# Kernel tuning notes

Measured on AMD Instinct MI355X. Metric: run time of the kernel, lower is better.

The kernel has to match this reference:

```python
import jax, jax.numpy as jnp
import numpy as np

N_NODES = 100000
N_EDGES = 1600000
DIM = 3
HID = 128
BN_EPS = 1e-5


def _bn(x, g, b):
    # BatchNorm1d, training-mode batch statistics (biased variance, like torch)
    m = jnp.mean(x, axis=0)
    v = jnp.var(x, axis=0)
    return (x - m) * jax.lax.rsqrt(v + BN_EPS) * g + b


def _gin_mlp(h, w1, b1, g1, be1, w2, b2, g2, be2, w3, b3):
    # Linear -> BN -> ReLU -> (Dropout: identity in eval) -> Linear -> BN -> ReLU -> Linear
    h = jax.nn.relu(_bn(h @ w1 + b1, g1, be1))
    h = jax.nn.relu(_bn(h @ w2 + b2, g2, be2))
    return h @ w3 + b3


def _gin_conv(x, src, dst, eps, mlp_params):
    # GINConv: mlp((1+eps)*x_i + sum_{j->i} x_j); scatter-add over edge targets
    agg = jax.ops.segment_sum(x[src], dst, num_segments=N_NODES)
    return _gin_mlp((1.0 + eps) * x + agg, *mlp_params)


def setup_inputs() -> dict:
    key = jax.random.key(0)
    ks = jax.random.split(key, 32)

    def w(k, shape, scale=0.05):
        return jax.random.normal(k, shape, dtype=jnp.float32) * scale

    inp = {}
    inp["coords"] = jax.random.normal(ks[0], (N_NODES, DIM), dtype=jnp.float32)
    inp["edge_index"] = jax.random.randint(ks[1], (2, N_EDGES), 0, N_NODES, dtype=jnp.int32)

    # GIN layer 0 MLP (dim -> hid -> hid -> hid)
    inp["g0_w1"] = w(ks[2], (DIM, HID)); inp["g0_b1"] = jnp.zeros((HID,), jnp.float32)
    inp["g0_g1"] = jnp.ones((HID,), jnp.float32); inp["g0_be1"] = jnp.zeros((HID,), jnp.float32)
    inp["g0_w2"] = w(ks[3], (HID, HID)); inp["g0_b2"] = jnp.zeros((HID,), jnp.float32)
    inp["g0_g2"] = jnp.ones((HID,), jnp.float32); inp["g0_be2"] = jnp.zeros((HID,), jnp.float32)
    inp["g0_w3"] = w(ks[4], (HID, HID)); inp["g0_b3"] = jnp.zeros((HID,), jnp.float32)
    inp["eps0"] = jnp.zeros((), jnp.float32)
    inp["bn0_g"] = jnp.ones((HID,), jnp.float32); inp["bn0_b"] = jnp.zeros((HID,), jnp.float32)

    # GIN layer 1 MLP (hid -> hid -> hid -> hid)
    inp["g1_w1"] = w(ks[5], (HID, HID)); inp["g1_b1"] = jnp.zeros((HID,), jnp.float32)
    inp["g1_g1"] = jnp.ones((HID,), jnp.float32); inp["g1_be1"] = jnp.zeros((HID,), jnp.float32)
    inp["g1_w2"] = w(ks[6], (HID, HID)); inp["g1_b2"] = jnp.zeros((HID,), jnp.float32)
    inp["g1_g2"] = jnp.ones((HID,), jnp.float32); inp["g1_be2"] = jnp.zeros((HID,), jnp.float32)
    inp["g1_w3"] = w(ks[7], (HID, HID)); inp["g1_b3"] = jnp.zeros((HID,), jnp.float32)
    inp["eps1"] = jnp.zeros((), jnp.float32)
    inp["bn1_g"] = jnp.ones((HID,), jnp.float32); inp["bn1_b"] = jnp.zeros((HID,), jnp.float32)

    # decoder MLP: (2*hid+1) -> hid -> hid//2 -> 1, sigmoid
    inp["d_w1"] = w(ks[8], (2 * HID + 1, HID)); inp["d_b1"] = jnp.zeros((HID,), jnp.float32)
    inp["d_g"] = jnp.ones((HID,), jnp.float32); inp["d_be"] = jnp.zeros((HID,), jnp.float32)
    inp["d_w2"] = w(ks[9], (HID, HID // 2)); inp["d_b2"] = jnp.zeros((HID // 2,), jnp.float32)
    inp["d_w3"] = w(ks[10], (HID // 2, 1)); inp["d_b3"] = jnp.zeros((1,), jnp.float32)
    return inp


def reference(coords, edge_index,
              g0_w1, g0_b1, g0_g1, g0_be1, g0_w2, g0_b2, g0_g2, g0_be2, g0_w3, g0_b3, eps0, bn0_g, bn0_b,
              g1_w1, g1_b1, g1_g1, g1_be1, g1_w2, g1_b2, g1_g2, g1_be2, g1_w3, g1_b3, eps1, bn1_g, bn1_b,
              d_w1, d_b1, d_g, d_be, d_w2, d_b2, d_w3, d_b3):
    node_0 = edge_index[0]
    node_1 = edge_index[1]

    mlp0 = (g0_w1, g0_b1, g0_g1, g0_be1, g0_w2, g0_b2, g0_g2, g0_be2, g0_w3, g0_b3)
    mlp1 = (g1_w1, g1_b1, g1_g1, g1_be1, g1_w2, g1_b2, g1_g2, g1_be2, g1_w3, g1_b3)

    x = _gin_conv(coords, node_0, node_1, eps0, mlp0)
    x = jax.nn.relu(_bn(x, bn0_g, bn0_b))
    x = _gin_conv(x, node_0, node_1, eps1, mlp1)
    x = jax.nn.relu(_bn(x, bn1_g, bn1_b))

    # edge_l_cntr branch: per-edge contour-length feature + endpoint concat
    l = jnp.linalg.norm(coords[node_1] - coords[node_0], axis=1, keepdims=True)  # [E,1]
    h = jnp.concatenate([x[node_0], x[node_1], l], axis=-1)  # [E, 2*hid+1]

    h = jax.nn.relu(_bn(h @ d_w1 + d_b1, d_g, d_be))
    h = jax.nn.relu(h @ d_w2 + d_b2)
    out = jax.nn.sigmoid((h @ d_w3 + d_b3).squeeze(-1))  # [E]
    return out
```

## Files before the change

### kernel.cpp

```cpp
#include <hip/hip_runtime.h>
#include <hip/hip_bf16.h>
#include <math.h>


typedef __attribute__((ext_vector_type(8))) __bf16 bf16x8;
typedef __attribute__((ext_vector_type(4))) float f32x4;

__device__ __forceinline__ unsigned int pack_bf16(float a, float b) {
    unsigned short ua = __builtin_bit_cast(unsigned short, __float2bfloat16(a));
    unsigned short ub = __builtin_bit_cast(unsigned short, __float2bfloat16(b));
    return (unsigned int)ua | ((unsigned int)ub << 16);
}
__device__ __forceinline__ float bflo(unsigned int u) {
    return __builtin_bit_cast(float, u << 16);
}
__device__ __forceinline__ float bfhi(unsigned int u) {
    return __builtin_bit_cast(float, u & 0xffff0000u);
}
__device__ __forceinline__ unsigned short bf16r(float a) {
    return __builtin_bit_cast(unsigned short, __float2bfloat16(a));
}


__global__ void hist_dst(const int* __restrict__ edst, int* __restrict__ cursor, int E) {
    int e = blockIdx.x * 256 + threadIdx.x;
    if (e < E) atomicAdd(&cursor[edst[e]], 1);
}

__global__ __launch_bounds__(1024) void scan_deg(const int* deg, int* rowoff, int* cursor, int N) {
    __shared__ int sums[1024];
    const int t = threadIdx.x;
    const int chunk = (N + 1023) >> 10;
    int lo = t * chunk, hi = lo + chunk;
    if (lo > N) lo = N;
    if (hi > N) hi = N;
    int s = 0;
    for (int i = lo; i < hi; ++i) s += deg[i];
    sums[t] = s;
    __syncthreads();
    for (int off = 1; off < 1024; off <<= 1) {
        int add = (t >= off) ? sums[t - off] : 0;
        __syncthreads();
        sums[t] += add;
        __syncthreads();
    }
    int run = sums[t] - s;
    for (int i = lo; i < hi; ++i) {
        int d = deg[i];
        rowoff[i] = run;
        cursor[i] = run;
        run += d;
    }
    if (t == 1023) rowoff[N] = sums[1023];
}

__global__ void fill_csr(const int* __restrict__ esrc, const int* __restrict__ edst,
                         const float* __restrict__ coords,
                         int* cursor, int* __restrict__ perm, int* __restrict__ dperm,
                         int* __restrict__ eperm, float* __restrict__ lperm, int E) {
    int e = blockIdx.x * 256 + threadIdx.x;
    if (e >= E) return;
    int s0 = esrc[e], d0 = edst[e];
    int pos = atomicAdd(&cursor[d0], 1);
    perm[pos] = s0;
    dperm[pos] = d0;
    eperm[pos] = e;
    float dx = coords[d0*3+0] - coords[s0*3+0];
    float dy = coords[d0*3+1] - coords[s0*3+1];
    float dz = coords[d0*3+2] - coords[s0*3+2];
    lperm[pos] = sqrtf(dx*dx + dy*dy + dz*dz);
}


__global__ void gather_coords(const float* __restrict__ coords,
                              const int* __restrict__ rowoff, const int* __restrict__ perm,
                              float* __restrict__ agg0, int N) {
    int i = blockIdx.x * 256 + threadIdx.x;
    if (i >= N) return;
    float ax = 0.f, ay = 0.f, az = 0.f;
    int b = rowoff[i], t = rowoff[i+1];
    for (int j = b; j < t; ++j) {
        int p = perm[j];
        ax += coords[p*3+0];
        ay += coords[p*3+1];
        az += coords[p*3+2];
    }
    agg0[i*3+0] = ax; agg0[i*3+1] = ay; agg0[i*3+2] = az;
}

__global__ __launch_bounds__(256) void gather_combine_bn(const unsigned short* __restrict__ x,
                                                         const int* __restrict__ rowoff,
                                                         const int* __restrict__ perm,
                                                         const float* __restrict__ st,
                                                         const float* __restrict__ g,
                                                         const float* __restrict__ be,
                                                         float invN,
                                                         const float* __restrict__ eps,
                                                         unsigned short* __restrict__ y, int N) {
    int node = blockIdx.x * 4 + (threadIdx.x >> 6);
    int lane = threadIdx.x & 63;
    if (node >= N) return;
    float ep = 1.f + *eps;
    int c0 = lane*2, c1 = c0 + 1;
    float m0 = st[c0]*invN, m1 = st[c1]*invN;
    float v0 = fmaxf(st[128+c0]*invN - m0*m0, 0.f);
    float v1 = fmaxf(st[128+c1]*invN - m1*m1, 0.f);
    float a0 = g[c0]*rsqrtf(v0 + 1e-5f), a1 = g[c1]*rsqrtf(v1 + 1e-5f);
    float sx = a0, sy = a1;
    float hx = be[c0] - m0*a0, hy = be[c1] - m1*a1;
    const unsigned int* x2 = (const unsigned int*)x;
    int b = rowoff[node], t = rowoff[node+1];
    float accx = 0.f, accy = 0.f;
    int j = b;
    for (; j + 2 <= t; j += 2) {
        unsigned int u0 = x2[(size_t)perm[j]*64 + lane];
        unsigned int u1 = x2[(size_t)perm[j+1]*64 + lane];
        accx += fmaxf(fmaf(bflo(u0), sx, hx), 0.f) + fmaxf(fmaf(bflo(u1), sx, hx), 0.f);
        accy += fmaxf(fmaf(bfhi(u0), sy, hy), 0.f) + fmaxf(fmaf(bfhi(u1), sy, hy), 0.f);
    }
    if (j < t) {
        unsigned int u = x2[(size_t)perm[j]*64 + lane];
        accx += fmaxf(fmaf(bflo(u), sx, hx), 0.f);
        accy += fmaxf(fmaf(bfhi(u), sy, hy), 0.f);
    }
    unsigned int uo = x2[(size_t)node*64 + lane];
    accx = fmaf(ep, fmaxf(fmaf(bflo(uo), sx, hx), 0.f), accx);
    accy = fmaf(ep, fmaxf(fmaf(bfhi(uo), sy, hy), 0.f), accy);
    ((unsigned int*)y)[(size_t)node*64 + lane] = pack_bf16(accx, accy);
}


__global__ __launch_bounds__(256) void lin0(const float* __restrict__ coords,
                                            const float* __restrict__ agg0,
                                            const float* __restrict__ W1,
                                            const float* __restrict__ b1,
                                            const float* __restrict__ eps0,
                                            unsigned short* __restrict__ t1,
                                            float* __restrict__ stats, int nrows) {
    int col = threadIdx.x & 127, half = threadIdx.x >> 7;
    float w0 = W1[col], w1 = W1[128+col], w2 = W1[256+col], bb = b1[col];
    float ep = 1.f + *eps0;
    float s = 0.f, q = 0.f;
    int r0 = blockIdx.x * 64;
    for (int i = 0; i < 32; ++i) {
        int row = r0 + half + 2*i;
        if (row < nrows) {
            float h0 = fmaf(ep, coords[row*3+0], agg0[row*3+0]);
            float h1 = fmaf(ep, coords[row*3+1], agg0[row*3+1]);
            float h2 = fmaf(ep, coords[row*3+2], agg0[row*3+2]);
            float v = fmaf(h0, w0, fmaf(h1, w1, fmaf(h2, w2, bb)));
            t1[row*128+col] = bf16r(v);
            s += v; q += v*v;
        }
    }
    __shared__ float red[512];
    red[half*128+col] = s;
    red[256 + half*128+col] = q;
    __syncthreads();
    if (threadIdx.x < 128) {
        atomicAdd(&stats[col],       red[col] + red[128+col]);
        atomicAdd(&stats[128+col],   red[256+col] + red[384+col]);
    }
}

__global__ void prep_w2(const float* __restrict__ W2, unsigned short* __restrict__ w2t) {
    int i = blockIdx.x * 256 + threadIdx.x;
    if (i >= 128*64) return;
    int k = i >> 6, c = i & 63;
    w2t[c*128 + k] = bf16r(W2[i]);
}

__global__ void prep_wT(const float* __restrict__ w0, const float* __restrict__ w1,
                        const float* __restrict__ w2, const float* __restrict__ w3,
                        const float* __restrict__ w4, const float* __restrict__ w5,
                        const float* __restrict__ w6, unsigned short* __restrict__ dst) {
    int m = blockIdx.y;
    const float* src = (m==0)?w0:(m==1)?w1:(m==2)?w2:(m==3)?w3:(m==4)?w4:(m==5)?w5:w6;
    int i = blockIdx.x * 256 + threadIdx.x;
    int k = i >> 7, c = i & 127;
    dst[m*16384 + c*128 + k] = bf16r(src[i]);
}

template<bool IN_BN, bool STATS>
__global__ __launch_bounds__(256) void gemm_mfma(const unsigned short* __restrict__ A,
                                                 const unsigned short* __restrict__ wT,
                                                 const float* __restrict__ bias,
                                                 const float* __restrict__ inst,
                                                 const float* __restrict__ bng,
                                                 const float* __restrict__ bnb,
                                                 float invCnt,
                                                 unsigned short* __restrict__ Cb,
                                                 float* __restrict__ stats, int nrows) {
    __shared__ int4 sAi[1024];
    __shared__ int4 sBi[2048];
    __shared__ float sred[2][4][128];
    char* sA = (char*)sAi;
    char* sB = (char*)sBi;
    float* sSC = &sred[0][0][0];
    float* sSH = &sred[0][1][0];
    const int tid = threadIdx.x;
    const int tile0 = blockIdx.x * 64;

    if (IN_BN) {
        if (tid < 128) {
            float m = inst[tid] * invCnt;
            float v = fmaxf(inst[128+tid] * invCnt - m*m, 0.f);
            float a = bng[tid] * rsqrtf(v + 1e-5f);
            sSC[tid] = a;
            sSH[tid] = bnb[tid] - m*a;
        }
        __syncthreads();
    }

    {
        const int4* src = (const int4*)wT;
        #pragma unroll
        for (int ii = 0; ii < 8; ++ii) {
            int s = tid + 256*ii;
            int col = s >> 4, k16 = s & 15;
            int byte = ((col << 8) + (k16 << 4)) ^ ((col & 7) << 4);
            *(int4*)(sB + byte) = src[s];
        }
    }
    {
        const int4* A4 = (const int4*)A;
        #pragma unroll
        for (int ii = 0; ii < 4; ++ii) {
            int s = tid + 256*ii;
            int r = s >> 4, k16 = s & 15;
            int row = tile0 + r;
            int4 raw = make_int4(0,0,0,0);
            if (row < nrows) raw = A4[(size_t)row*16 + k16];
            if (IN_BN) {
                float4 sa = ((const float4*)sSC)[k16*2];
                float4 sb = ((const float4*)sSC)[k16*2+1];
                float4 ha = ((const float4*)sSH)[k16*2];
                float4 hb = ((const float4*)sSH)[k16*2+1];
                unsigned int ux = raw.x, uy = raw.y, uz = raw.z, uw = raw.w;
                float e0 = fmaxf(fmaf(bflo(ux), sa.x, ha.x), 0.f);
                float e1 = fmaxf(fmaf(bfhi(ux), sa.y, ha.y), 0.f);
                float e2 = fmaxf(fmaf(bflo(uy), sa.z, ha.z), 0.f);
                float e3 = fmaxf(fmaf(bfhi(uy), sa.w, ha.w), 0.f);
                float e4 = fmaxf(fmaf(bflo(uz), sb.x, hb.x), 0.f);
                float e5 = fmaxf(fmaf(bfhi(uz), sb.y, hb.y), 0.f);
                float e6 = fmaxf(fmaf(bflo(uw), sb.z, hb.z), 0.f);
                float e7 = fmaxf(fmaf(bfhi(uw), sb.w, hb.w), 0.f);
                raw.x = (int)pack_bf16(e0, e1);
                raw.y = (int)pack_bf16(e2, e3);
                raw.z = (int)pack_bf16(e4, e5);
                raw.w = (int)pack_bf16(e6, e7);
            }
            int byte = ((r << 8) + (k16 << 4)) ^ ((r & 7) << 4);
            *(int4*)(sA + byte) = raw;
        }
    }
    __syncthreads();

    const int l = tid & 63;
    const int w = tid >> 6;
    const int arow = (w << 4) + (l & 15);
    const int kbase = (l >> 4) << 3;
    f32x4 accv[8];
    #pragma unroll
    for (int c = 0; c < 8; ++c) accv[c] = (f32x4){0.f, 0.f, 0.f, 0.f};

    #pragma unroll
    for (int t = 0; t < 4; ++t) {
        int k0 = t*32 + kbase;
        int abyte = ((arow << 8) + (k0 << 1)) ^ ((arow & 7) << 4);
        bf16x8 af = __builtin_bit_cast(bf16x8, *(const int4*)(sA + abyte));
        #pragma unroll
        for (int c = 0; c < 8; ++c) {
            int bcol = (c << 4) + (l & 15);
            int bbyte = ((bcol << 8) + (k0 << 1)) ^ ((bcol & 7) << 4);
            bf16x8 bf = __builtin_bit_cast(bf16x8, *(const int4*)(sB + bbyte));
            accv[c] = __builtin_amdgcn_mfma_f32_16x16x32_bf16(af, bf, accv[c], 0, 0, 0);
        }
    }

    const int rj = (l >> 4) << 2;
    float lsum[8], lsq[8];
    #pragma unroll
    for (int c = 0; c < 8; ++c) {
        int col = (c << 4) + (l & 15);
        float bv = bias ? bias[col] : 0.f;
        f32x4 a = accv[c];
        float s = 0.f, q = 0.f;
        #pragma unroll
        for (int j = 0; j < 4; ++j) {
            int row = tile0 + (w << 4) + rj + j;
            float o = a[j] + bv;
            if (row < nrows) {
                Cb[(size_t)row*128 + col] = bf16r(o);
                if (STATS) { s += o; q += o*o; }
            }
        }
        lsum[c] = s; lsq[c] = q;
    }
    if (STATS) {
        #pragma unroll
        for (int c = 0; c < 8; ++c) {
            lsum[c] += __shfl_xor(lsum[c], 16, 64);
            lsum[c] += __shfl_xor(lsum[c], 32, 64);
            lsq[c]  += __shfl_xor(lsq[c], 16, 64);
            lsq[c]  += __shfl_xor(lsq[c], 32, 64);
        }
        __syncthreads();
        if ((l >> 4) == 0) {
            #pragma unroll
            for (int c = 0; c < 8; ++c) {
                int col = (c << 4) + l;
                sred[0][w][col] = lsum[c];
                sred[1][w][col] = lsq[c];
            }
        }
        __syncthreads();
        if (tid < 128) {
            float s = sred[0][0][tid] + sred[0][1][tid] + sred[0][2][tid] + sred[0][3][tid];
            float q = sred[1][0][tid] + sred[1][1][tid] + sred[1][2][tid] + sred[1][3][tid];
            atomicAdd(&stats[tid], s);
            atomicAdd(&stats[128 + tid], q);
        }
    }
}

__global__ __launch_bounds__(256) void csr_stats(const unsigned short* __restrict__ ya,
                                                 const unsigned short* __restrict__ yb,
                                                 const int* __restrict__ rowoff,
                                                 const int* __restrict__ perm,
                                                 const float* __restrict__ lperm,
                                                 const float* __restrict__ wl,
                                                 const float* __restrict__ b1,
                                                 float* __restrict__ stats, int N, int nspan) {
    int w = blockIdx.x * 4 + (threadIdx.x >> 6);
    int lane = threadIdx.x & 63;
    const unsigned int* ya2 = (const unsigned int*)ya;
    const unsigned int* yb2 = (const unsigned int*)yb;
    float2 wl2 = ((const float2*)wl)[lane];
    float2 b12 = ((const float2*)b1)[lane];
    float2 s = make_float2(0.f, 0.f), q = make_float2(0.f, 0.f);
    int i0 = w * nspan;
    int i1 = i0 + nspan; if (i1 > N) i1 = N;
    for (int i = i0; i < i1; ++i) {
        unsigned int ub = yb2[(size_t)i*64 + lane];
        float ybx = bflo(ub), yby = bfhi(ub);
        int b = rowoff[i], t = rowoff[i+1];
        int j = b;
        for (; j + 2 <= t; j += 2) {
            int p0 = perm[j], p1 = perm[j+1];
            float l0 = lperm[j], l1 = lperm[j+1];
            unsigned int ua0 = ya2[(size_t)p0*64 + lane];
            unsigned int ua1 = ya2[(size_t)p1*64 + lane];
            float z0x = bflo(ua0) + ybx + fmaf(l0, wl2.x, b12.x);
            float z0y = bfhi(ua0) + yby + fmaf(l0, wl2.y, b12.y);
            float z1x = bflo(ua1) + ybx + fmaf(l1, wl2.x, b12.x);
            float z1y = bfhi(ua1) + yby + fmaf(l1, wl2.y, b12.y);
            s.x += z0x + z1x; s.y += z0y + z1y;
            q.x += fmaf(z0x, z0x, z1x*z1x);
            q.y += fmaf(z0y, z0y, z1y*z1y);
        }
        if (j < t) {
            int p = perm[j];
            float lv = lperm[j];
            unsigned int ua = ya2[(size_t)p*64 + lane];
            float zx = bflo(ua) + ybx + fmaf(lv, wl2.x, b12.x);
            float zy = bfhi(ua) + yby + fmaf(lv, wl2.y, b12.y);
            s.x += zx; s.y += zy;
            q.x += zx*zx; q.y += zy*zy;
        }
    }
    __shared__ float red[1024];
    int wv = threadIdx.x >> 6;
    red[wv*128 + lane*2]       = s.x;
    red[wv*128 + lane*2 + 1]   = s.y;
    red[512 + wv*128 + lane*2]     = q.x;
    red[512 + wv*128 + lane*2 + 1] = q.y;
    __syncthreads();
    if (threadIdx.x < 128) {
        int c = threadIdx.x;
        float ss = red[c] + red[128+c] + red[256+c] + red[384+c];
        float qq = red[512+c] + red[640+c] + red[768+c] + red[896+c];
        atomicAdd(&stats[c], ss);
        atomicAdd(&stats[128+c], qq);
    }
}

__global__ __launch_bounds__(256) void decoder_fused(const unsigned short* __restrict__ ya,
                                                     const unsigned short* __restrict__ yb,
                                                     const float* __restrict__ lperm,
                                                     const int* __restrict__ perm,
                                                     const int* __restrict__ dperm,
                                                     const int* __restrict__ eperm,
                                                     const float* __restrict__ wl,
                                                     const float* __restrict__ b1,
                                                     const float* __restrict__ st6,
                                                     const float* __restrict__ dg,
                                                     const float* __restrict__ dbe,
                                                     float invE,
                                                     const unsigned short* __restrict__ w2t,
                                                     const float* __restrict__ b2,
                                                     const float* __restrict__ w3,
                                                     const float* __restrict__ b3p,
                                                     float* __restrict__ out, int E) {
    __shared__ int4 sAB[2048];
    char* sA = (char*)sAB;
    char* sB = (char*)sAB + 16384;
    const int tid = threadIdx.x;
    const int tile0 = blockIdx.x * 64;

    {
        const int4* src = (const int4*)w2t;
        #pragma unroll
        for (int ii = 0; ii < 4; ++ii) {
            int s = tid + 256*ii;
            int col = s >> 4, k16 = s & 15;
            int byte = ((col << 8) + (k16 << 4)) ^ ((col & 7) << 4);
            *(int4*)(sB + byte) = src[s];
        }
    }
    {
        const int c4 = tid & 31;
        const int rb = tid >> 5;
        float4 wv = ((const float4*)wl)[c4];
        float4 bb = ((const float4*)b1)[c4];
        float4 s4, t4;
        {
            int cb = c4 * 4;
            #pragma unroll
            for (int j = 0; j < 4; ++j) {
                float m = st6[cb+j] * invE;
                float v = fmaxf(st6[128+cb+j] * invE - m*m, 0.f);
                float a = dg[cb+j] * rsqrtf(v + 1e-5f);
                ((float*)&s4)[j] = a;
                ((float*)&t4)[j] = dbe[cb+j] - m*a;
            }
        }
        const uint2* ya2 = (const uint2*)ya;
        const uint2* yb2 = (const uint2*)yb;
        #pragma unroll
        for (int i = 0; i < 8; ++i) {
            int r = rb + 8*i;
            int row = tile0 + r;
            float4 v = make_float4(0.f, 0.f, 0.f, 0.f);
            if (row < E) {
                int s0 = perm[row], d0 = dperm[row];
                float lv = lperm[row];
                uint2 ua = ya2[(size_t)s0*32 + c4];
                uint2 ubv = yb2[(size_t)d0*32 + c4];
                float vax = bflo(ua.x), vay = bfhi(ua.x), vaz = bflo(ua.y), vaw = bfhi(ua.y);
                float vbx = bflo(ubv.x), vby = bfhi(ubv.x), vbz = bflo(ubv.y), vbw = bfhi(ubv.y);
                v.x = fmaxf(fmaf(vax + vbx + fmaf(lv, wv.x, bb.x), s4.x, t4.x), 0.f);
                v.y = fmaxf(fmaf(vay + vby + fmaf(lv, wv.y, bb.y), s4.y, t4.y), 0.f);
                v.z = fmaxf(fmaf(vaz + vbz + fmaf(lv, wv.z, bb.z), s4.z, t4.z), 0.f);
                v.w = fmaxf(fmaf(vaw + vbw + fmaf(lv, wv.w, bb.w), s4.w, t4.w), 0.f);
            }
            uint2 pk;
            pk.x = pack_bf16(v.x, v.y);
            pk.y = pack_bf16(v.z, v.w);
            int byte = ((r << 8) + (c4 << 3)) ^ ((r & 7) << 4);
            *(uint2*)(sA + byte) = pk;
        }
    }
    __syncthreads();

    const int l = tid & 63;
    const int w = tid >> 6;
    const int arow = (w << 4) + (l & 15);
    const int kbase = (l >> 4) << 3;
    f32x4 accv[4];
    #pragma unroll
    for (int c = 0; c < 4; ++c) accv[c] = (f32x4){0.f, 0.f, 0.f, 0.f};

    #pragma unroll
    for (int t = 0; t < 4; ++t) {
        int k0 = t*32 + kbase;
        int abyte = ((arow << 8) + (k0 << 1)) ^ ((arow & 7) << 4);
        bf16x8 af = __builtin_bit_cast(bf16x8, *(const int4*)(sA + abyte));
        #pragma unroll
        for (int c = 0; c < 4; ++c) {
            int bcol = (c << 4) + (l & 15);
            int bbyte = ((bcol << 8) + (k0 << 1)) ^ ((bcol & 7) << 4);
            bf16x8 bf = __builtin_bit_cast(bf16x8, *(const int4*)(sB + bbyte));
            accv[c] = __builtin_amdgcn_mfma_f32_16x16x32_bf16(af, bf, accv[c], 0, 0, 0);
        }
    }

    float p0 = 0.f, p1 = 0.f, p2 = 0.f, p3 = 0.f;
    #pragma unroll
    for (int c = 0; c < 4; ++c) {
        int col = (c << 4) + (l & 15);
        float b2c = b2[col], w3c = w3[col];
        f32x4 a = accv[c];
        p0 = fmaf(fmaxf(a[0] + b2c, 0.f), w3c, p0);
        p1 = fmaf(fmaxf(a[1] + b2c, 0.f), w3c, p1);
        p2 = fmaf(fmaxf(a[2] + b2c, 0.f), w3c, p2);
        p3 = fmaf(fmaxf(a[3] + b2c, 0.f), w3c, p3);
    }
    #pragma unroll
    for (int m = 1; m < 16; m <<= 1) {
        p0 += __shfl_xor(p0, m, 64);
        p1 += __shfl_xor(p1, m, 64);
        p2 += __shfl_xor(p2, m, 64);
        p3 += __shfl_xor(p3, m, 64);
    }
    if ((l & 15) == 0) {
        float b3v = b3p[0];
        int rbase = tile0 + (w << 4) + ((l >> 4) << 2);
        float pj[4] = {p0, p1, p2, p3};
        #pragma unroll
        for (int j = 0; j < 4; ++j) {
            int row = rbase + j;
            if (row < E) out[eperm[row]] = 1.f / (1.f + expf(-(pj[j] + b3v)));
        }
    }
}


extern "C" void kernel_launch(void* const* d_in, const int* in_sizes, int n_in,
                              void* d_out, int out_size, void* d_ws, size_t ws_size,
                              hipStream_t stream) {
    const int N = in_sizes[0] / 3;
    const int E = in_sizes[1] / 2;

    const float* coords = (const float*)d_in[0];
    const int*   ei     = (const int*)d_in[1];
    const int*   esrc = ei;
    const int*   edst = ei + E;
    const float* g0_w1 = (const float*)d_in[2];
    const float* g0_b1 = (const float*)d_in[3];
    const float* g0_g1 = (const float*)d_in[4];
    const float* g0_be1= (const float*)d_in[5];
    const float* g0_w2 = (const float*)d_in[6];
    const float* g0_b2 = (const float*)d_in[7];
    const float* g0_g2 = (const float*)d_in[8];
    const float* g0_be2= (const float*)d_in[9];
    const float* g0_w3 = (const float*)d_in[10];
    const float* g0_b3 = (const float*)d_in[11];
    const float* eps0  = (const float*)d_in[12];
    const float* bn0_g = (const float*)d_in[13];
    const float* bn0_b = (const float*)d_in[14];
    const float* g1_w1 = (const float*)d_in[15];
    const float* g1_b1 = (const float*)d_in[16];
    const float* g1_g1 = (const float*)d_in[17];
    const float* g1_be1= (const float*)d_in[18];
    const float* g1_w2 = (const float*)d_in[19];
    const float* g1_b2 = (const float*)d_in[20];
    const float* g1_g2 = (const float*)d_in[21];
    const float* g1_be2= (const float*)d_in[22];
    const float* g1_w3 = (const float*)d_in[23];
    const float* g1_b3 = (const float*)d_in[24];
    const float* eps1  = (const float*)d_in[25];
    const float* bn1_g = (const float*)d_in[26];
    const float* bn1_b = (const float*)d_in[27];
    const float* d_w1  = (const float*)d_in[28];
    const float* d_b1  = (const float*)d_in[29];
    const float* d_g   = (const float*)d_in[30];
    const float* d_be  = (const float*)d_in[31];
    const float* d_w2  = (const float*)d_in[32];
    const float* d_b2  = (const float*)d_in[33];
    const float* d_w3  = (const float*)d_in[34];
    const float* d_b3  = (const float*)d_in[35];

    float* ws = (float*)d_ws;
    const size_t NF = (size_t)N * 128;
    float* buf0 = ws;
    float* buf1 = ws + NF;
    float* buf2 = ws + 2*NF;
    float* agg0 = ws + 3*NF;
    float* stats= agg0 + (size_t)N*3;
    float* scsh = stats + 7*256;
    float* lperm = scsh + 7*256;
    int*   cursor = (int*)(lperm + E);
    int*   rowoff = cursor + N;
    int*   perm   = rowoff + N + 1;
    int*   dperm  = perm + E;
    int*   eperm  = dperm + E;
    unsigned short* w2t = (unsigned short*)(eperm + E);
    unsigned short* wT  = w2t + 64*128;

    unsigned short* b0 = (unsigned short*)buf0;
    unsigned short* b1b = (unsigned short*)buf1;
    unsigned short* b2b = (unsigned short*)buf2;

    float* out = (float*)d_out;

    const float* wl = d_w1 + 256*128;

    #define STATSK(k) (stats + (k)*256)
    #define WT(m) (wT + (m)*16384)

    const int rowTiles = (N + 63) / 64;
    const int edgeTiles = (E + 63) / 64;
    const int eBlocks = (E + 255) / 256;
    const float invN = 1.f / (float)N;
    const float invE = 1.f / (float)E;
    const int nWaves = 2048 * 4;
    const int nspan = (N + nWaves - 1) / nWaves;

    hipMemsetAsync(stats, 0, 7*256 * sizeof(float), stream);
    hipMemsetAsync(cursor, 0, (size_t)N * sizeof(int), stream);

    hist_dst<<<eBlocks, 256, 0, stream>>>(edst, cursor, E);
    scan_deg<<<1, 1024, 0, stream>>>(cursor, rowoff, cursor, N);
    fill_csr<<<eBlocks, 256, 0, stream>>>(esrc, edst, coords, cursor, perm, dperm, eperm, lperm, E);
    prep_w2<<<32, 256, 0, stream>>>(d_w2, w2t);
    prep_wT<<<dim3(64, 7), 256, 0, stream>>>(g0_w2, g0_w3, g1_w1, g1_w2, g1_w3,
                                             d_w1, d_w1 + 128*128, wT);

    gather_coords<<<(N + 255)/256, 256, 0, stream>>>(coords, rowoff, perm, agg0, N);
    lin0<<<rowTiles, 256, 0, stream>>>(coords, agg0, g0_w1, g0_b1, eps0, b0, STATSK(0), N);
    gemm_mfma<true,true><<<rowTiles, 256, 0, stream>>>(
        b0, WT(0), g0_b2, STATSK(0), g0_g1, g0_be1, invN, b1b, STATSK(1), N);
    gemm_mfma<true,true><<<rowTiles, 256, 0, stream>>>(
        b1b, WT(1), g0_b3, STATSK(1), g0_g2, g0_be2, invN, b2b, STATSK(2), N);

    gather_combine_bn<<<(N + 3)/4, 256, 0, stream>>>(
        b2b, rowoff, perm, STATSK(2), bn0_g, bn0_b, invN, eps1, b0, N);
    gemm_mfma<false,true><<<rowTiles, 256, 0, stream>>>(
        b0, WT(2), g1_b1, nullptr, nullptr, nullptr, 0.f, b1b, STATSK(3), N);
    gemm_mfma<true,true><<<rowTiles, 256, 0, stream>>>(
        b1b, WT(3), g1_b2, STATSK(3), g1_g1, g1_be1, invN, b2b, STATSK(4), N);
    gemm_mfma<true,true><<<rowTiles, 256, 0, stream>>>(
        b2b, WT(4), g1_b3, STATSK(4), g1_g2, g1_be2, invN, b0, STATSK(5), N);

    gemm_mfma<true,false><<<rowTiles, 256, 0, stream>>>(
        b0, WT(5), nullptr, STATSK(5), bn1_g, bn1_b, invN, b1b, nullptr, N);
    gemm_mfma<true,false><<<rowTiles, 256, 0, stream>>>(
        b0, WT(6), nullptr, STATSK(5), bn1_g, bn1_b, invN, b2b, nullptr, N);
    csr_stats<<<2048, 256, 0, stream>>>(b1b, b2b, rowoff, perm, lperm, wl, d_b1,
                                        STATSK(6), N, nspan);
    decoder_fused<<<edgeTiles, 256, 0, stream>>>(b1b, b2b, lperm, perm, dperm, eperm,
                                                 wl, d_b1, STATSK(6), d_g, d_be, invE,
                                                 w2t, d_b2, d_w3, d_b3, out, E);
}
```

Baseline: 1.385 ms.

## Unroll CSR gathers by four and double decoder tile to 128 edges

The neighbor gather loops in gather_combine_bn and csr_stats are unrolled from two to four so more independent loads are in flight per wave. The decoder kernel now handles 128 edges per block with 512 threads, so the shared copy of the w2 weights is loaded once per 128 edges instead of once per 64. The A tile in shared memory holds all 128 rows while B keeps its own buffer. This trades more registers per thread and a larger shared-memory footprint for fewer redundant weight loads and better latency hiding. The decoder indexing changes are only partly visible and must match the new tile shape.

```diff
diff --git a/kernel.cpp b/kernel.cpp
--- a/kernel.cpp
+++ b/kernel.cpp
@@ -105,20 +105,23 @@
     float m0 = st[c0]*invN, m1 = st[c1]*invN;
     float v0 = fmaxf(st[128+c0]*invN - m0*m0, 0.f);
     float v1 = fmaxf(st[128+c1]*invN - m1*m1, 0.f);
-    float a0 = g[c0]*rsqrtf(v0 + 1e-5f), a1 = g[c1]*rsqrtf(v1 + 1e-5f);
-    float sx = a0, sy = a1;
-    float hx = be[c0] - m0*a0, hy = be[c1] - m1*a1;
+    float sx = g[c0]*rsqrtf(v0 + 1e-5f), sy = g[c1]*rsqrtf(v1 + 1e-5f);
+    float hx = be[c0] - m0*sx, hy = be[c1] - m1*sy;
     const unsigned int* x2 = (const unsigned int*)x;
     int b = rowoff[node], t = rowoff[node+1];
     float accx = 0.f, accy = 0.f;
     int j = b;
-    for (; j + 2 <= t; j += 2) {
+    for (; j + 4 <= t; j += 4) {
         unsigned int u0 = x2[(size_t)perm[j]*64 + lane];
         unsigned int u1 = x2[(size_t)perm[j+1]*64 + lane];
-        accx += fmaxf(fmaf(bflo(u0), sx, hx), 0.f) + fmaxf(fmaf(bflo(u1), sx, hx), 0.f);
-        accy += fmaxf(fmaf(bfhi(u0), sy, hy), 0.f) + fmaxf(fmaf(bfhi(u1), sy, hy), 0.f);
-    }
-    if (j < t) {
+        unsigned int u2 = x2[(size_t)perm[j+2]*64 + lane];
+        unsigned int u3 = x2[(size_t)perm[j+3]*64 + lane];
+        accx += fmaxf(fmaf(bflo(u0), sx, hx), 0.f) + fmaxf(fmaf(bflo(u1), sx, hx), 0.f)
+              + fmaxf(fmaf(bflo(u2), sx, hx), 0.f) + fmaxf(fmaf(bflo(u3), sx, hx), 0.f);
+        accy += fmaxf(fmaf(bfhi(u0), sy, hy), 0.f) + fmaxf(fmaf(bfhi(u1), sy, hy), 0.f)
+              + fmaxf(fmaf(bfhi(u2), sy, hy), 0.f) + fmaxf(fmaf(bfhi(u3), sy, hy), 0.f);
+    }
+    for (; j < t; ++j) {
         unsigned int u = x2[(size_t)perm[j]*64 + lane];
         accx += fmaxf(fmaf(bflo(u), sx, hx), 0.f);
         accy += fmaxf(fmaf(bfhi(u), sy, hy), 0.f);
@@ -346,20 +349,27 @@
         float ybx = bflo(ub), yby = bfhi(ub);
         int b = rowoff[i], t = rowoff[i+1];
         int j = b;
-        for (; j + 2 <= t; j += 2) {
-            int p0 = perm[j], p1 = perm[j+1];
-            float l0 = lperm[j], l1 = lperm[j+1];
+        for (; j + 4 <= t; j += 4) {
+            int p0 = perm[j], p1 = perm[j+1], p2 = perm[j+2], p3 = perm[j+3];
+            float l0 = lperm[j], l1 = lperm[j+1], l2 = lperm[j+2], l3 = lperm[j+3];
             unsigned int ua0 = ya2[(size_t)p0*64 + lane];
             unsigned int ua1 = ya2[(size_t)p1*64 + lane];
+            unsigned int ua2 = ya2[(size_t)p2*64 + lane];
+            unsigned int ua3 = ya2[(size_t)p3*64 + lane];
             float z0x = bflo(ua0) + ybx + fmaf(l0, wl2.x, b12.x);
             float z0y = bfhi(ua0) + yby + fmaf(l0, wl2.y, b12.y);
             float z1x = bflo(ua1) + ybx + fmaf(l1, wl2.x, b12.x);
             float z1y = bfhi(ua1) + yby + fmaf(l1, wl2.y, b12.y);
-            s.x += z0x + z1x; s.y += z0y + z1y;
-            q.x += fmaf(z0x, z0x, z1x*z1x);
-            q.y += fmaf(z0y, z0y, z1y*z1y);
-        }
-        if (j < t) {
+            float z2x = bflo(ua2) + ybx + fmaf(l2, wl2.x, b12.x);
+            float z2y = bfhi(ua2) + yby + fmaf(l2, wl2.y, b12.y);
+            float z3x = bflo(ua3) + ybx + fmaf(l3, wl2.x, b12.x);
+            float z3y = bfhi(ua3) + yby + fmaf(l3, wl2.y, b12.y);
+            s.x += (z0x + z1x) + (z2x + z3x);
+            s.y += (z0y + z1y) + (z2y + z3y);
+            q.x += fmaf(z0x, z0x, z1x*z1x) + fmaf(z2x, z2x, z3x*z3x);
+            q.y += fmaf(z0y, z0y, z1y*z1y) + fmaf(z2y, z2y, z3y*z3y);
+        }
+        for (; j < t; ++j) {
             int p = perm[j];
             float lv = lperm[j];
             unsigned int ua = ya2[(size_t)p*64 + lane];
@@ -385,7 +395,7 @@
     }
 }
 
-__global__ __launch_bounds__(256) void decoder_fused(const unsigned short* __restrict__ ya,
+__global__ __launch_bounds__(512) void decoder_fused(const unsigned short* __restrict__ ya,
                                                      const unsigned short* __restrict__ yb,
                                                      const float* __restrict__ lperm,
                                                      const int* __restrict__ perm,
@@ -402,17 +412,18 @@
                                                      const float* __restrict__ w3,
                                                      const float* __restrict__ b3p,
                                                      float* __restrict__ out, int E) {
-    __shared__ int4 sAB[2048];
-    char* sA = (char*)sAB;
-    char* sB = (char*)sAB + 16384;
+    __shared__ int4 sAi[2048];
+    __shared__ int4 sBi[1024];
+    char* sA = (char*)sAi;
+    char* sB = (char*)sBi;
     const int tid = threadIdx.x;
-    const int tile0 = blockIdx.x * 64;
+    const int tile0 = blockIdx.x * 128;
 
     {
         const int4* src = (const int4*)w2t;
         #pragma unroll
-        for (int ii = 0; ii < 4; ++ii) {
-            int s = tid + 256*ii;
+        for (int ii = 0; ii < 2; ++ii) {
+            int s = tid + 512*ii;
             int col = s >> 4, k16 = s & 15;
             int byte = ((col << 8) + (k16 << 4)) ^ ((col & 7) << 4);
             *(int4*)(sB + byte) = src[s];
@@ -439,7 +450,7 @@
         const uint2* yb2 = (const uint2*)yb;
         #pragma unroll
         for (int i = 0; i < 8; ++i) {
-            int r = rb + 8*i;
+            int r = rb + 16*i;
             int row = tile0 + r;
             float4 v = make_float4(0.f, 0.f, 0.f, 0.f);
             if (row < E) {
@@ -590,7 +601,7 @@
     #define WT(m) (wT + (m)*16384)
 
     const int rowTiles = (N + 63) / 64;
-    const int edgeTiles = (E + 63) / 64;
+    const int edgeTiles128 = (E + 127) / 128;
     const int eBlocks = (E + 255) / 256;
     const float invN = 1.f / (float)N;
     const float invE = 1.f / (float)E;
@@ -629,7 +640,7 @@
         b0, WT(6), nullptr, STATSK(5), bn1_g, bn1_b, invN, b2b, nullptr, N);
     csr_stats<<<2048, 256, 0, stream>>>(b1b, b2b, rowoff, perm, lperm, wl, d_b1,
                                         STATSK(6), N, nspan);
-    decoder_fused<<<edgeTiles, 256, 0, stream>>>(b1b, b2b, lperm, perm, dperm, eperm,
-                                                 wl, d_b1, STATSK(6), d_g, d_be, invE,
-                                                 w2t, d_b2, d_w3, d_b3, out, E);
-}
+    decoder_fused<<<edgeTiles128, 512, 0, stream>>>(b1b, b2b, lperm, perm, dperm, eperm,
+                                                    wl, d_b1, STATSK(6), d_g, d_be, invE,
+                                                    w2t, d_b2, d_w3, d_b3, out, E);
+}
```

After: 1.291 ms. 1.07x faster.
